# Performance work log

Measured on AMD Instinct MI355X. Metric: run time of the kernel, lower is better.

The kernel has to match this reference:

```python
import jax, jax.numpy as jnp
import numpy as np

D = 2048      # hidden_size
H = 16        # num_attention_heads
KV = 4        # num_key_value_heads
HD = 128      # head_dim
E = 16        # num_experts
TOPK = 2      # num_experts_per_tok
I = 768       # moe_intermediate_size
EPS = 1e-6
THETA = 1000000.0


def rms_norm(x, w, eps=EPS):
    x32 = x.astype(jnp.float32)
    y = x32 * jax.lax.rsqrt(jnp.mean(x32 * x32, axis=-1, keepdims=True) + eps)
    return (y.astype(x.dtype)) * w


def rotate_half(x):
    x1, x2 = jnp.split(x, 2, axis=-1)
    return jnp.concatenate([-x2, x1], axis=-1)


def rope_cos_sin(position_ids):
    inv_freq = 1.0 / (THETA ** (jnp.arange(0, HD, 2, dtype=jnp.float32) / HD))
    ang = position_ids.astype(jnp.float32)[..., None] * inv_freq   # [B,S,HD/2]
    emb = jnp.concatenate([ang, ang], axis=-1)                     # [B,S,HD]
    return jnp.cos(emb)[:, None, :, :], jnp.sin(emb)[:, None, :, :]  # [B,1,S,HD]


def setup_inputs() -> dict:
    key = jax.random.key(0)
    ks = jax.random.split(key, 10)
    s = 0.02
    B, S = 1, 1024
    return {
        "hidden_states": jax.random.normal(ks[0], (B, S, D), jnp.float32),
        "ln1_w": jnp.ones((D,), jnp.float32),
        "ln2_w": jnp.ones((D,), jnp.float32),
        "qn_w": jnp.ones((HD,), jnp.float32),
        "kn_w": jnp.ones((HD,), jnp.float32),
        "Wq": jax.random.normal(ks[1], (H * HD, D), jnp.float32) * s,
        "Wk": jax.random.normal(ks[2], (KV * HD, D), jnp.float32) * s,
        "Wv": jax.random.normal(ks[3], (KV * HD, D), jnp.float32) * s,
        "Wo": jax.random.normal(ks[4], (D, H * HD), jnp.float32) * s,
        "gate_w": jax.random.normal(ks[5], (E, D), jnp.float32) * s,
        "Wg": jax.random.normal(ks[6], (E, I, D), jnp.float32) * s,
        "Wu": jax.random.normal(ks[7], (E, I, D), jnp.float32) * s,
        "Wd": jax.random.normal(ks[8], (E, D, I), jnp.float32) * s,
        "position_ids": jnp.arange(S, dtype=jnp.int32)[None, :],
    }


def attention(h, qn_w, kn_w, Wq, Wk, Wv, Wo, position_ids):
    B, S, _ = h.shape
    q = (h @ Wq.T).reshape(B, S, H, HD)
    k = (h @ Wk.T).reshape(B, S, KV, HD)
    v = (h @ Wv.T).reshape(B, S, KV, HD)
    q = rms_norm(q, qn_w).transpose(0, 2, 1, 3)   # [B,H,S,HD]
    k = rms_norm(k, kn_w).transpose(0, 2, 1, 3)   # [B,KV,S,HD]
    v = v.transpose(0, 2, 1, 3)
    cos, sin = rope_cos_sin(position_ids)
    q = q * cos + rotate_half(q) * sin
    k = k * cos + rotate_half(k) * sin
    # repeat_kv (GQA): expand KV heads to H heads
    rep = H // KV
    k = jnp.repeat(k, rep, axis=1)
    v = jnp.repeat(v, rep, axis=1)
    scale = HD ** -0.5
    scores = jnp.einsum('bhqd,bhkd->bhqk', q, k) * scale
    probs = jax.nn.softmax(scores.astype(jnp.float32), axis=-1).astype(q.dtype)
    out = jnp.einsum('bhqk,bhkd->bhqd', probs, v)
    out = out.transpose(0, 2, 1, 3).reshape(B, S, H * HD)
    return out @ Wo.T


def moe(h, gate_w, Wg, Wu, Wd):
    B, S, _ = h.shape
    x = h.reshape(-1, D)                                  # [T,D]
    T = x.shape[0]
    logits = x @ gate_w.T                                 # [T,E]
    probs = jax.nn.softmax(logits.astype(jnp.float32), axis=-1)
    w, sel = jax.lax.top_k(probs, TOPK)                   # [T,K]
    w = w / jnp.sum(w, axis=-1, keepdims=True)            # norm_topk_prob
    combine = jnp.zeros((T, E), jnp.float32).at[jnp.arange(T)[:, None], sel].add(w)
    g = jnp.einsum('td,eid->tei', x, Wg)                  # [T,E,I]
    u = jnp.einsum('td,eid->tei', x, Wu)
    a = jax.nn.silu(g) * u
    y = jnp.einsum('tei,edi->ted', a, Wd)                 # [T,E,D]
    out = jnp.einsum('ted,te->td', y, combine.astype(x.dtype))
    return out.reshape(B, S, D)


def reference(hidden_states, ln1_w, ln2_w, qn_w, kn_w, Wq, Wk, Wv, Wo, gate_w, Wg, Wu, Wd, position_ids):
    # pre-attn RMSNorm -> bidirectional GQA attention -> residual
    residual = hidden_states
    h = rms_norm(hidden_states, ln1_w)
    h = residual + attention(h, qn_w, kn_w, Wq, Wk, Wv, Wo, position_ids)
    # post-attn RMSNorm -> top-k sparse MoE -> residual
    residual = h
    h2 = rms_norm(h, ln2_w)
    return residual + moe(h2, gate_w, Wg, Wu, Wd)
```

## Files before the change

kernel.cpp:

```cpp
#include <hip/hip_runtime.h>
#include <hip/hip_bf16.h>
#include <math.h>

#define D 2048
#define NH 16
#define NKV 4
#define HD 128
#define NE 16
#define NI 768
#define S 1024
#define EPS 1e-6f

typedef __attribute__((ext_vector_type(8))) short bf16x8;
typedef __attribute__((ext_vector_type(4))) float f32x4;

__device__ __forceinline__ float wave_reduce_sum64(float v) {
    for (int off = 32; off; off >>= 1) v += __shfl_xor(v, off, 64);
    return v;
}

__device__ __forceinline__ unsigned short f2bf(float f) {
    unsigned int x = __float_as_uint(f);
    x += 0x7FFFu + ((x >> 16) & 1u);
    return (unsigned short)(x >> 16);
}

__device__ __forceinline__ bf16x8 pack8(const float4 a, const float4 b) {
    bf16x8 r;
    r[0] = (short)f2bf(a.x); r[1] = (short)f2bf(a.y);
    r[2] = (short)f2bf(a.z); r[3] = (short)f2bf(a.w);
    r[4] = (short)f2bf(b.x); r[5] = (short)f2bf(b.y);
    r[6] = (short)f2bf(b.z); r[7] = (short)f2bf(b.w);
    return r;
}

__global__ void rmsnorm_kernel(const float* __restrict__ x, const float* __restrict__ w,
                               float* __restrict__ y, unsigned short* __restrict__ yb) {
    int t = blockIdx.x;
    const float* xr = x + (size_t)t * D;
    float* yr = y + (size_t)t * D;
    float v[8];
    float ss = 0.f;
#pragma unroll
    for (int m = 0; m < 8; ++m) {
        v[m] = xr[threadIdx.x + 256 * m];
        ss += v[m] * v[m];
    }
    ss = wave_reduce_sum64(ss);
    __shared__ float wsum[4];
    if ((threadIdx.x & 63) == 0) wsum[threadIdx.x >> 6] = ss;
    __syncthreads();
    float tot = wsum[0] + wsum[1] + wsum[2] + wsum[3];
    float r = rsqrtf(tot / (float)D + EPS);
#pragma unroll
    for (int m = 0; m < 8; ++m) {
        int d = threadIdx.x + 256 * m;
        float val = v[m] * r * w[d];
        yr[d] = val;
        if (yb) yb[(size_t)t * D + d] = f2bf(val);
    }
}

__global__ __launch_bounds__(256) void mfma_gemm_kernel(
    const float* __restrict__ A, int lda,
    const float* __restrict__ W, int ldw,
    float* __restrict__ C, int ldc,
    const float* __restrict__ R, float* __restrict__ C2,
    int M, int N, int K)
{
    int m0 = blockIdx.y * 64;
    int n0 = blockIdx.x * 64;

    __shared__ unsigned short As[64 * 64];
    __shared__ unsigned short Bs[64 * 64];

    int tid = threadIdx.x;
    int srow = tid >> 2;
    int scol = (tid & 3) * 16;

    const float* ap = A + (size_t)(m0 + srow) * lda + scol;
    const float* wp = W + (size_t)(n0 + srow) * ldw + scol;

    int wlo[2];
#pragma unroll
    for (int u = 0; u < 2; ++u) {
        int g = (tid & 3) * 2 + u;
        wlo[u] = srow * 64 + (g ^ (srow & 7)) * 8;
    }

    int wid = tid >> 6, lane = tid & 63;
    int wm = wid >> 1, wn = wid & 1;
    int l16 = lane & 15, lhi = lane >> 4;

    int ra[2][2], rb[2][2];
#pragma unroll
    for (int f = 0; f < 2; ++f) {
        int rowa = wm * 32 + f * 16 + l16;
        int rowb = wn * 32 + f * 16 + l16;
#pragma unroll
        for (int kh = 0; kh < 2; ++kh) {
            ra[f][kh] = rowa * 64 + (((kh * 4 + lhi) ^ (rowa & 7))) * 8;
            rb[f][kh] = rowb * 64 + (((kh * 4 + lhi) ^ (rowb & 7))) * 8;
        }
    }

    f32x4 acc[2][2] = {};
    float4 av[4], wv[4];

    auto ldt = [&](int k0) {
#pragma unroll
        for (int u = 0; u < 4; ++u) {
            av[u] = *(const float4*)(ap + k0 + u * 4);
            wv[u] = *(const float4*)(wp + k0 + u * 4);
        }
    };

    ldt(0);
    for (int k0 = 0; k0 < K; k0 += 64) {
        bf16x8 pa0 = pack8(av[0], av[1]);
        bf16x8 pa1 = pack8(av[2], av[3]);
        bf16x8 pw0 = pack8(wv[0], wv[1]);
        bf16x8 pw1 = pack8(wv[2], wv[3]);
        __syncthreads();
        *(bf16x8*)(As + wlo[0]) = pa0;
        *(bf16x8*)(As + wlo[1]) = pa1;
        *(bf16x8*)(Bs + wlo[0]) = pw0;
        *(bf16x8*)(Bs + wlo[1]) = pw1;
        __syncthreads();
        if (k0 + 64 < K) ldt(k0 + 64);
#pragma unroll
        for (int kh = 0; kh < 2; ++kh) {
            bf16x8 af0 = *(const bf16x8*)(As + ra[0][kh]);
            bf16x8 af1 = *(const bf16x8*)(As + ra[1][kh]);
            bf16x8 bf0 = *(const bf16x8*)(Bs + rb[0][kh]);
            bf16x8 bf1 = *(const bf16x8*)(Bs + rb[1][kh]);
            acc[0][0] = __builtin_amdgcn_mfma_f32_16x16x32_bf16(af0, bf0, acc[0][0], 0, 0, 0);
            acc[0][1] = __builtin_amdgcn_mfma_f32_16x16x32_bf16(af0, bf1, acc[0][1], 0, 0, 0);
            acc[1][0] = __builtin_amdgcn_mfma_f32_16x16x32_bf16(af1, bf0, acc[1][0], 0, 0, 0);
            acc[1][1] = __builtin_amdgcn_mfma_f32_16x16x32_bf16(af1, bf1, acc[1][1], 0, 0, 0);
        }
    }

#pragma unroll
    for (int mi = 0; mi < 2; ++mi) {
#pragma unroll
        for (int r = 0; r < 4; ++r) {
            int grow = m0 + wm * 32 + mi * 16 + lhi * 4 + r;
#pragma unroll
            for (int ni = 0; ni < 2; ++ni) {
                int gcol = n0 + wn * 32 + ni * 16 + l16;
                float v = acc[mi][ni][r];
                if (R) v += R[(size_t)grow * ldc + gcol];
                C[(size_t)grow * ldc + gcol] = v;
                if (C2) C2[(size_t)grow * ldc + gcol] = v;
            }
        }
    }
}

__global__ __launch_bounds__(256) void qkv_gemm_kernel(
    const float* __restrict__ A,
    const float* __restrict__ Wq, const float* __restrict__ Wk, const float* __restrict__ Wv,
    float* __restrict__ C)
{
    int m0 = blockIdx.y * 64;
    int n0 = blockIdx.x * 64;

    const float* W;
    int wr0;
    if (n0 < 2048)      { W = Wq; wr0 = n0; }
    else if (n0 < 2560) { W = Wk; wr0 = n0 - 2048; }
    else                { W = Wv; wr0 = n0 - 2560; }

    __shared__ unsigned short As[64 * 64];
    __shared__ unsigned short Bs[64 * 64];

    int tid = threadIdx.x;
    int srow = tid >> 2;
    int scol = (tid & 3) * 16;

    const float* ap = A + (size_t)(m0 + srow) * D + scol;
    const float* wp = W + (size_t)(wr0 + srow) * D + scol;

    int wlo[2];
#pragma unroll
    for (int u = 0; u < 2; ++u) {
        int g = (tid & 3) * 2 + u;
        wlo[u] = srow * 64 + (g ^ (srow & 7)) * 8;
    }

    int wid = tid >> 6, lane = tid & 63;
    int wm = wid >> 1, wn = wid & 1;
    int l16 = lane & 15, lhi = lane >> 4;

    int ra[2][2], rb[2][2];
#pragma unroll
    for (int f = 0; f < 2; ++f) {
        int rowa = wm * 32 + f * 16 + l16;
        int rowb = wn * 32 + f * 16 + l16;
#pragma unroll
        for (int kh = 0; kh < 2; ++kh) {
            ra[f][kh] = rowa * 64 + (((kh * 4 + lhi) ^ (rowa & 7))) * 8;
            rb[f][kh] = rowb * 64 + (((kh * 4 + lhi) ^ (rowb & 7))) * 8;
        }
    }

    f32x4 acc[2][2] = {};
    float4 av[4], wv[4];

    auto ldt = [&](int k0) {
#pragma unroll
        for (int u = 0; u < 4; ++u) {
            av[u] = *(const float4*)(ap + k0 + u * 4);
            wv[u] = *(const float4*)(wp + k0 + u * 4);
        }
    };

    ldt(0);
    for (int k0 = 0; k0 < D; k0 += 64) {
        bf16x8 pa0 = pack8(av[0], av[1]);
        bf16x8 pa1 = pack8(av[2], av[3]);
        bf16x8 pw0 = pack8(wv[0], wv[1]);
        bf16x8 pw1 = pack8(wv[2], wv[3]);
        __syncthreads();
        *(bf16x8*)(As + wlo[0]) = pa0;
        *(bf16x8*)(As + wlo[1]) = pa1;
        *(bf16x8*)(Bs + wlo[0]) = pw0;
        *(bf16x8*)(Bs + wlo[1]) = pw1;
        __syncthreads();
        if (k0 + 64 < D) ldt(k0 + 64);
#pragma unroll
        for (int kh = 0; kh < 2; ++kh) {
            bf16x8 af0 = *(const bf16x8*)(As + ra[0][kh]);
            bf16x8 af1 = *(const bf16x8*)(As + ra[1][kh]);
            bf16x8 bf0 = *(const bf16x8*)(Bs + rb[0][kh]);
            bf16x8 bf1 = *(const bf16x8*)(Bs + rb[1][kh]);
            acc[0][0] = __builtin_amdgcn_mfma_f32_16x16x32_bf16(af0, bf0, acc[0][0], 0, 0, 0);
            acc[0][1] = __builtin_amdgcn_mfma_f32_16x16x32_bf16(af0, bf1, acc[0][1], 0, 0, 0);
            acc[1][0] = __builtin_amdgcn_mfma_f32_16x16x32_bf16(af1, bf0, acc[1][0], 0, 0, 0);
            acc[1][1] = __builtin_amdgcn_mfma_f32_16x16x32_bf16(af1, bf1, acc[1][1], 0, 0, 0);
        }
    }

#pragma unroll
    for (int mi = 0; mi < 2; ++mi) {
#pragma unroll
        for (int r = 0; r < 4; ++r) {
            int grow = m0 + wm * 32 + mi * 16 + lhi * 4 + r;
#pragma unroll
            for (int ni = 0; ni < 2; ++ni) {
                int gcol = n0 + wn * 32 + ni * 16 + l16;
                C[(size_t)grow * 3072 + gcol] = acc[mi][ni][r];
            }
        }
    }
}

__global__ __launch_bounds__(256) void moe_mlp_kernel(
    const unsigned short* __restrict__ h2b,
    const float* __restrict__ Wg, const float* __restrict__ Wu,
    const int* __restrict__ cnt, const int* __restrict__ elist,
    unsigned short* __restrict__ abuf)
{
    int e = blockIdx.z;
    int me = cnt[e];
    int m0 = blockIdx.y * 64;
    if (m0 >= me) return;
    int n0 = blockIdx.x * 16;

    __shared__ unsigned short As[64 * 64];
    __shared__ unsigned short Gs[16 * 64];
    __shared__ unsigned short Us[16 * 64];
    __shared__ int ridx[64];

    int tid = threadIdx.x;
    const int* idx = elist + e * S;
    if (tid < 64) ridx[tid] = (m0 + tid < me) ? idx[m0 + tid] : -1;
    __syncthreads();

    int arow_i = tid >> 2;
    int acolg = (tid & 3) * 16;
    int rva = ridx[arow_i];
    const unsigned short* arow = (rva >= 0) ? (h2b + (size_t)(rva >> 1) * D + acolg) : nullptr;
    int wa[2];
#pragma unroll
    for (int u = 0; u < 2; ++u) {
        int g = (tid & 3) * 2 + u;
        wa[u] = arow_i * 64 + (g ^ (arow_i & 7)) * 8;
    }

    int tl = tid & 127;
    int bwrow = tl >> 3;
    int bg8 = tl & 7;
    const float* bp = ((tid < 128) ? Wg : Wu) + ((size_t)e * NI + n0 + bwrow) * D + bg8 * 8;
    unsigned short* bs = (tid < 128) ? Gs : Us;
    int wbo = bwrow * 64 + (bg8 ^ (bwrow & 7)) * 8;

    int wid = tid >> 6, lane = tid & 63;
    int l16 = lane & 15, lhi = lane >> 4;

    int raoff[2], rboff[2];
    {
        int rowa = wid * 16 + l16;
#pragma unroll
        for (int kh = 0; kh < 2; ++kh) {
            raoff[kh] = rowa * 64 + (((kh * 4 + lhi) ^ (rowa & 7))) * 8;
            rboff[kh] = l16 * 64 + (((kh * 4 + lhi) ^ (l16 & 7))) * 8;
        }
    }

    f32x4 accg = {}, accu = {};
    bf16x8 av[2];
    float4 bv[2];

    auto ldt = [&](int k0) {
        if (arow) {
            av[0] = *(const bf16x8*)(arow + k0);
            av[1] = *(const bf16x8*)(arow + k0 + 8);
        } else {
            bf16x8 z = {};
            av[0] = z; av[1] = z;
        }
        bv[0] = *(const float4*)(bp + k0);
        bv[1] = *(const float4*)(bp + k0 + 4);
    };

    ldt(0);
    for (int k0 = 0; k0 < D; k0 += 64) {
        bf16x8 a0s = av[0], a1s = av[1];
        bf16x8 pb = pack8(bv[0], bv[1]);
        __syncthreads();
        *(bf16x8*)(As + wa[0]) = a0s;
        *(bf16x8*)(As + wa[1]) = a1s;
        *(bf16x8*)(bs + wbo) = pb;
        __syncthreads();
        if (k0 + 64 < D) ldt(k0 + 64);
#pragma unroll
        for (int kh = 0; kh < 2; ++kh) {
            bf16x8 a = *(const bf16x8*)(As + raoff[kh]);
            bf16x8 bgf = *(const bf16x8*)(Gs + rboff[kh]);
            bf16x8 buf = *(const bf16x8*)(Us + rboff[kh]);
            accg = __builtin_amdgcn_mfma_f32_16x16x32_bf16(a, bgf, accg, 0, 0, 0);
            accu = __builtin_amdgcn_mfma_f32_16x16x32_bf16(a, buf, accu, 0, 0, 0);
        }
    }

#pragma unroll
    for (int r = 0; r < 4; ++r) {
        int lrow = wid * 16 + lhi * 4 + r;
        int rv = ridx[lrow];
        if (rv < 0) continue;
        float g = accg[r];
        float u = accu[r];
        float a = g / (1.f + __expf(-g)) * u;
        abuf[(size_t)rv * NI + n0 + l16] = f2bf(a);
    }
}

__global__ __launch_bounds__(256) void moe_down_kernel(
    const unsigned short* __restrict__ abuf, const float* __restrict__ Wd,
    const int* __restrict__ cnt, const int* __restrict__ elist,
    const float* __restrict__ wbuf, float* __restrict__ out)
{
    int e = blockIdx.z;
    int me = cnt[e];
    int m0 = blockIdx.y * 64;
    if (m0 >= me) return;
    int n0 = blockIdx.x * 16;

    __shared__ unsigned short As[64 * 64];
    __shared__ unsigned short Bs[16 * 64];
    __shared__ int ridx[64];

    int tid = threadIdx.x;
    const int* idx = elist + e * S;
    if (tid < 64) ridx[tid] = (m0 + tid < me) ? idx[m0 + tid] : -1;
    __syncthreads();

    int arow_i = tid >> 2;
    int acolg = (tid & 3) * 16;
    int rva = ridx[arow_i];
    const unsigned short* arow = (rva >= 0) ? (abuf + (size_t)rva * NI + acolg) : nullptr;
    int wa[2];
#pragma unroll
    for (int u = 0; u < 2; ++u) {
        int g = (tid & 3) * 2 + u;
        wa[u] = arow_i * 64 + (g ^ (arow_i & 7)) * 8;
    }

    int tl = tid & 127;
    int bwrow = tl >> 3;
    int bg8 = tl & 7;
    const float* bp = Wd + ((size_t)e * D + n0 + bwrow) * NI + bg8 * 8;
    int wbo = bwrow * 64 + (bg8 ^ (bwrow & 7)) * 8;
    bool doB = tid < 128;

    int wid = tid >> 6, lane = tid & 63;
    int l16 = lane & 15, lhi = lane >> 4;

    int raoff[2], rboff[2];
    {
        int rowa = wid * 16 + l16;
#pragma unroll
        for (int kh = 0; kh < 2; ++kh) {
            raoff[kh] = rowa * 64 + (((kh * 4 + lhi) ^ (rowa & 7))) * 8;
            rboff[kh] = l16 * 64 + (((kh * 4 + lhi) ^ (l16 & 7))) * 8;
        }
    }

    f32x4 acc = {};
    bf16x8 av[2];
    float4 bv[2];

    auto ldt = [&](int k0) {
        if (arow) {
            av[0] = *(const bf16x8*)(arow + k0);
            av[1] = *(const bf16x8*)(arow + k0 + 8);
        } else {
            bf16x8 z = {};
            av[0] = z; av[1] = z;
        }
        if (doB) {
            bv[0] = *(const float4*)(bp + k0);
            bv[1] = *(const float4*)(bp + k0 + 4);
        }
    };

    ldt(0);
    for (int k0 = 0; k0 < NI; k0 += 64) {
        bf16x8 a0s = av[0], a1s = av[1];
        bf16x8 pb = pack8(bv[0], bv[1]);
        __syncthreads();
        *(bf16x8*)(As + wa[0]) = a0s;
        *(bf16x8*)(As + wa[1]) = a1s;
        if (doB) *(bf16x8*)(Bs + wbo) = pb;
        __syncthreads();
        if (k0 + 64 < NI) ldt(k0 + 64);
#pragma unroll
        for (int kh = 0; kh < 2; ++kh) {
            bf16x8 a = *(const bf16x8*)(As + raoff[kh]);
            bf16x8 b = *(const bf16x8*)(Bs + rboff[kh]);
            acc = __builtin_amdgcn_mfma_f32_16x16x32_bf16(a, b, acc, 0, 0, 0);
        }
    }

#pragma unroll
    for (int r = 0; r < 4; ++r) {
        int lrow = wid * 16 + lhi * 4 + r;
        int rv = ridx[lrow];
        if (rv < 0) continue;
        float w = wbuf[rv];
        atomicAdd(out + (size_t)(rv >> 1) * D + n0 + l16, w * acc[r]);
    }
}

__global__ void qkrope_bf16_kernel(const float* __restrict__ qkvb,
                                   const float* __restrict__ qn_w, const float* __restrict__ kn_w,
                                   const int* __restrict__ pos_ids,
                                   unsigned short* __restrict__ qbh, unsigned short* __restrict__ kbh)
{
    int t = blockIdx.x;
    int h = blockIdx.y;
    int d = threadIdx.x;
    const float* base;
    const float* w;
    unsigned short* ob;
    float scale;
    if (h < NH) {
        base = qkvb + (size_t)t * 3072 + h * HD; w = qn_w;
        ob = qbh + (size_t)t * D + h * HD; scale = 0.08838834764831845f;
    } else {
        base = qkvb + (size_t)t * 3072 + 2048 + (h - NH) * HD; w = kn_w;
        ob = kbh + (size_t)t * (NKV * HD) + (h - NH) * HD; scale = 1.0f;
    }
    float x1 = base[d], x2 = base[d + 64];
    float ss = wave_reduce_sum64(x1 * x1 + x2 * x2);
    float r = rsqrtf(ss / (float)HD + EPS);
    float n1 = x1 * r * w[d];
    float n2 = x2 * r * w[d + 64];
    float pos = (float)pos_ids[t];
    float freq = powf(1000000.0f, -(float)d * (1.0f / 64.0f));
    float ang = pos * freq;
    float c, s;
    sincosf(ang, &s, &c);
    ob[d]      = f2bf((n1 * c - n2 * s) * scale);
    ob[d + 64] = f2bf((n2 * c + n1 * s) * scale);
}

__global__ void vtrans_kernel(const float* __restrict__ qkvb, unsigned short* __restrict__ vbt)
{
    __shared__ unsigned short tile[64][65];
    int s0 = blockIdx.x * 64, d0 = blockIdx.y * 64, kvh = blockIdx.z;
    int tid = threadIdx.x;
    {
        int i = tid >> 2;
        int j4 = (tid & 3) * 16;
        const float* src = qkvb + (size_t)(s0 + i) * 3072 + 2560 + kvh * HD + d0 + j4;
#pragma unroll
        for (int u = 0; u < 4; ++u) {
            float4 f = *(const float4*)(src + u * 4);
            tile[i][j4 + u * 4 + 0] = f2bf(f.x);
            tile[i][j4 + u * 4 + 1] = f2bf(f.y);
            tile[i][j4 + u * 4 + 2] = f2bf(f.z);
            tile[i][j4 + u * 4 + 3] = f2bf(f.w);
        }
    }
    __syncthreads();
    {
        int j = tid >> 2;
        int i4 = (tid & 3) * 16;
        bf16x8 o0, o1;
#pragma unroll
        for (int u = 0; u < 8; ++u) {
            o0[u] = (short)tile[i4 + u][j];
            o1[u] = (short)tile[i4 + 8 + u][j];
        }
        unsigned short* dst = vbt + ((size_t)kvh * HD + d0 + j) * S + s0 + i4;
        *(bf16x8*)(dst) = o0;
        *(bf16x8*)(dst + 8) = o1;
    }
}

__global__ __launch_bounds__(256) void flash_attn_mfma_kernel(
    const unsigned short* __restrict__ qbh, const unsigned short* __restrict__ kbh,
    const unsigned short* __restrict__ vbt, float* __restrict__ o)
{
    int qt = blockIdx.x;
    int h  = blockIdx.y;
    int kvh = h >> 2;

    __shared__ unsigned short Qs[64 * 128];
    __shared__ unsigned short Ks[64 * 128];
    __shared__ unsigned short Vs[128 * 64];
    __shared__ unsigned short Ps[4][16 * 72];

    int tid = threadIdx.x;
    int wid = tid >> 6, lane = tid & 63;
    int l16 = lane & 15, lhi = lane >> 4;

    {
        int r = tid >> 2;
        int gb = (tid & 3) * 4;
        const unsigned short* src = qbh + (size_t)(qt * 64 + r) * D + h * HD;
#pragma unroll
        for (int u = 0; u < 4; ++u) {
            int g = gb + u;
            bf16x8 val = *(const bf16x8*)(src + g * 8);
            *(bf16x8*)(Qs + r * 128 + (g ^ (r & 7)) * 8) = val;
        }
    }

    int qrow = wid * 16 + l16;
    int qoff[4];
#pragma unroll
    for (int kh = 0; kh < 4; ++kh)
        qoff[kh] = qrow * 128 + (((kh * 4 + lhi) ^ (qrow & 7))) * 8;

    float mreg[4], lreg[4];
#pragma unroll
    for (int r = 0; r < 4; ++r) { mreg[r] = -3.0e38f; lreg[r] = 0.f; }
    f32x4 oacc[8] = {};

    for (int kt = 0; kt < S / 64; ++kt) {
        __syncthreads();
        {
            int r = tid >> 2;
            int gb = (tid & 3) * 4;
            const unsigned short* src = kbh + (size_t)(kt * 64 + r) * (NKV * HD) + kvh * HD;
#pragma unroll
            for (int u = 0; u < 4; ++u) {
                int g = gb + u;
                bf16x8 val = *(const bf16x8*)(src + g * 8);
                *(bf16x8*)(Ks + r * 128 + (g ^ (r & 7)) * 8) = val;
            }
        }
        {
            int r = tid >> 1;
            int gb = (tid & 1) * 4;
            const unsigned short* src = vbt + ((size_t)kvh * HD + r) * S + kt * 64;
#pragma unroll
            for (int u = 0; u < 4; ++u) {
                int g = gb + u;
                bf16x8 val = *(const bf16x8*)(src + g * 8);
                *(bf16x8*)(Vs + r * 64 + (g ^ (r & 7)) * 8) = val;
            }
        }
        __syncthreads();

        bf16x8 qa[4];
#pragma unroll
        for (int kh = 0; kh < 4; ++kh) qa[kh] = *(const bf16x8*)(Qs + qoff[kh]);
        f32x4 sc[4] = {};
#pragma unroll
        for (int nf = 0; nf < 4; ++nf) {
            int krow = nf * 16 + l16;
#pragma unroll
            for (int kh = 0; kh < 4; ++kh) {
                bf16x8 kf = *(const bf16x8*)(Ks + krow * 128 + (((kh * 4 + lhi) ^ (krow & 7))) * 8);
                sc[nf] = __builtin_amdgcn_mfma_f32_16x16x32_bf16(qa[kh], kf, sc[nf], 0, 0, 0);
            }
        }

        float corr[4];
#pragma unroll
        for (int r = 0; r < 4; ++r) {
            float tmax = fmaxf(fmaxf(sc[0][r], sc[1][r]), fmaxf(sc[2][r], sc[3][r]));
            tmax = fmaxf(tmax, __shfl_xor(tmax, 1, 64));
            tmax = fmaxf(tmax, __shfl_xor(tmax, 2, 64));
            tmax = fmaxf(tmax, __shfl_xor(tmax, 4, 64));
            tmax = fmaxf(tmax, __shfl_xor(tmax, 8, 64));
            float mn = fmaxf(mreg[r], tmax);
            corr[r] = __expf(mreg[r] - mn);
            mreg[r] = mn;
            float psum = 0.f;
#pragma unroll
            for (int nf = 0; nf < 4; ++nf) {
                float p = __expf(sc[nf][r] - mn);
                sc[nf][r] = p;
                psum += p;
            }
            psum += __shfl_xor(psum, 1, 64);
            psum += __shfl_xor(psum, 2, 64);
            psum += __shfl_xor(psum, 4, 64);
            psum += __shfl_xor(psum, 8, 64);
            lreg[r] = lreg[r] * corr[r] + psum;
        }
#pragma unroll
        for (int fb = 0; fb < 8; ++fb)
#pragma unroll
            for (int r = 0; r < 4; ++r) oacc[fb][r] *= corr[r];

#pragma unroll
        for (int nf = 0; nf < 4; ++nf)
#pragma unroll
            for (int r = 0; r < 4; ++r)
                Ps[wid][(lhi * 4 + r) * 72 + nf * 16 + l16] = f2bf(sc[nf][r]);

        bf16x8 pa[2];
#pragma unroll
        for (int k2 = 0; k2 < 2; ++k2)
            pa[k2] = *(const bf16x8*)(&Ps[wid][l16 * 72 + k2 * 32 + lhi * 8]);

#pragma unroll
        for (int fb = 0; fb < 8; ++fb) {
            int vrow = fb * 16 + l16;
#pragma unroll
            for (int k2 = 0; k2 < 2; ++k2) {
                bf16x8 vf = *(const bf16x8*)(Vs + vrow * 64 + (((k2 * 4 + lhi) ^ (vrow & 7))) * 8);
                oacc[fb] = __builtin_amdgcn_mfma_f32_16x16x32_bf16(pa[k2], vf, oacc[fb], 0, 0, 0);
            }
        }
    }

    float linv[4];
#pragma unroll
    for (int r = 0; r < 4; ++r) linv[r] = 1.f / lreg[r];
#pragma unroll
    for (int fb = 0; fb < 8; ++fb) {
#pragma unroll
        for (int r = 0; r < 4; ++r) {
            int row = qt * 64 + wid * 16 + lhi * 4 + r;
            o[(size_t)row * D + h * HD + fb * 16 + l16] = oacc[fb][r] * linv[r];
        }
    }
}

__global__ void gate_kernel(const float* __restrict__ x, const float* __restrict__ gw,
                            float* __restrict__ wbuf, int* __restrict__ cnt, int* __restrict__ elist)
{
    int t = blockIdx.x;
    int g = threadIdx.x >> 4, j = threadIdx.x & 15;
    const float* xr = x + (size_t)t * D;
    const float* gr = gw + (size_t)g * D;
    float p = 0.f;
    for (int m = 0; m < D / 16; ++m) p += xr[j + 16 * m] * gr[j + 16 * m];
    for (int off = 8; off; off >>= 1) p += __shfl_down(p, off, 64);
    __shared__ float lg[NE];
    if (j == 0) lg[g] = p;
    __syncthreads();
    if (threadIdx.x == 0) {
        float l0 = -1e30f; int i0 = 0;
        for (int e = 0; e < NE; ++e) if (lg[e] > l0) { l0 = lg[e]; i0 = e; }
        float l1 = -1e30f; int i1 = 0;
        for (int e = 0; e < NE; ++e) if (e != i0 && lg[e] > l1) { l1 = lg[e]; i1 = e; }
        float rr = expf(l1 - l0);
        wbuf[t * 2 + 0] = 1.f / (1.f + rr);
        wbuf[t * 2 + 1] = rr / (1.f + rr);
        int s0 = atomicAdd(&cnt[i0], 1); elist[i0 * S + s0] = t * 2;
        int s1 = atomicAdd(&cnt[i1], 1); elist[i1 * S + s1] = t * 2 + 1;
    }
}

extern "C" void kernel_launch(void* const* d_in, const int* in_sizes, int n_in,
                              void* d_out, int out_size, void* d_ws, size_t ws_size,
                              hipStream_t stream)
{
    const float* hidden = (const float*)d_in[0];
    const float* ln1 = (const float*)d_in[1];
    const float* ln2 = (const float*)d_in[2];
    const float* qn  = (const float*)d_in[3];
    const float* kn  = (const float*)d_in[4];
    const float* Wq  = (const float*)d_in[5];
    const float* Wk  = (const float*)d_in[6];
    const float* Wv  = (const float*)d_in[7];
    const float* Wo  = (const float*)d_in[8];
    const float* gw  = (const float*)d_in[9];
    const float* Wg  = (const float*)d_in[10];
    const float* Wu  = (const float*)d_in[11];
    const float* Wd  = (const float*)d_in[12];
    const int*   pos = (const int*)d_in[13];

    float* ws    = (float*)d_ws;
    float* h1    = ws;
    float* qkvb  = h1 + 2097152;
    float* attn  = qkvb + 3145728;
    float* hattn = attn + 2097152;
    float* h2    = hattn + 2097152;
    float* h2bf  = h2 + 2097152;
    float* wbuf  = h2bf + 1048576;
    int*   cnt   = (int*)(wbuf + 2048);
    int*   elist = cnt + 16;

    unsigned short* qbh = (unsigned short*)h1;
    unsigned short* kbh = (unsigned short*)(h1 + 1048576);
    unsigned short* vbt = (unsigned short*)(h1 + 1310720);
    unsigned short* abuf = (unsigned short*)attn;
    unsigned short* h2b  = (unsigned short*)h2bf;
    float* out   = (float*)d_out;

    hipMemsetAsync(cnt, 0, NE * sizeof(int), stream);

    rmsnorm_kernel<<<S, 256, 0, stream>>>(hidden, ln1, h1, nullptr);
    qkv_gemm_kernel<<<dim3(48, 16), 256, 0, stream>>>(h1, Wq, Wk, Wv, qkvb);
    qkrope_bf16_kernel<<<dim3(S, NH + NKV), 64, 0, stream>>>(qkvb, qn, kn, pos, qbh, kbh);
    vtrans_kernel<<<dim3(S / 64, HD / 64, NKV), 256, 0, stream>>>(qkvb, vbt);
    flash_attn_mfma_kernel<<<dim3(S / 64, NH), 256, 0, stream>>>(qbh, kbh, vbt, attn);
    mfma_gemm_kernel<<<dim3(32, 16), 256, 0, stream>>>(attn, D, Wo, D, hattn, D, hidden, out, S, 2048, D);
    rmsnorm_kernel<<<S, 256, 0, stream>>>(hattn, ln2, h2, h2b);
    gate_kernel<<<S, 256, 0, stream>>>(h2, gw, wbuf, cnt, elist);
    moe_mlp_kernel<<<dim3(NI / 16, 16, NE), 256, 0, stream>>>(h2b, Wg, Wu, cnt, elist, abuf);
    moe_down_kernel<<<dim3(D / 16, 16, NE), 256, 0, stream>>>(abuf, Wd, cnt, elist, wbuf, out);
}
```

Baseline: 342.3 us.

## Double-buffer LDS tiles in all GEMM kernels with one barrier per stage

Converts the generic, QKV, MoE gate/up and MoE down GEMM kernels to ping-pong LDS buffers with two register sets of prefetched global loads, processing two K-tiles per loop iteration. This removes one of the two __syncthreads per K-step and issues the next global load earlier, so memory latency overlaps the MFMAs. In exchange it doubles LDS use and adds prefetch registers, which may lower occupancy. It also assumes K is a multiple of 128, which holds for 2048 and 768.

```diff
diff --git a/kernel.cpp b/kernel.cpp
--- a/kernel.cpp
+++ b/kernel.cpp
@@ -71,8 +71,8 @@
     int m0 = blockIdx.y * 64;
     int n0 = blockIdx.x * 64;
 
-    __shared__ unsigned short As[64 * 64];
-    __shared__ unsigned short Bs[64 * 64];
+    __shared__ unsigned short As[2][64 * 64];
+    __shared__ unsigned short Bs[2][64 * 64];
 
     int tid = threadIdx.x;
     int srow = tid >> 2;
@@ -105,40 +105,49 @@
     }
 
     f32x4 acc[2][2] = {};
-    float4 av[4], wv[4];
-
-    auto ldt = [&](int k0) {
+    float4 avA[4], wvA[4], avB[4], wvB[4];
+
+    auto ldt = [&](float4* av, float4* wv, int k0) {
 #pragma unroll
         for (int u = 0; u < 4; ++u) {
             av[u] = *(const float4*)(ap + k0 + u * 4);
             wv[u] = *(const float4*)(wp + k0 + u * 4);
         }
     };
-
-    ldt(0);
-    for (int k0 = 0; k0 < K; k0 += 64) {
+    auto stage = [&](const float4* av, const float4* wv, int b) {
         bf16x8 pa0 = pack8(av[0], av[1]);
         bf16x8 pa1 = pack8(av[2], av[3]);
         bf16x8 pw0 = pack8(wv[0], wv[1]);
         bf16x8 pw1 = pack8(wv[2], wv[3]);
-        __syncthreads();
-        *(bf16x8*)(As + wlo[0]) = pa0;
-        *(bf16x8*)(As + wlo[1]) = pa1;
-        *(bf16x8*)(Bs + wlo[0]) = pw0;
-        *(bf16x8*)(Bs + wlo[1]) = pw1;
-        __syncthreads();
-        if (k0 + 64 < K) ldt(k0 + 64);
+        *(bf16x8*)(&As[b][wlo[0]]) = pa0;
+        *(bf16x8*)(&As[b][wlo[1]]) = pa1;
+        *(bf16x8*)(&Bs[b][wlo[0]]) = pw0;
+        *(bf16x8*)(&Bs[b][wlo[1]]) = pw1;
+    };
+    auto domfma = [&](int b) {
 #pragma unroll
         for (int kh = 0; kh < 2; ++kh) {
-            bf16x8 af0 = *(const bf16x8*)(As + ra[0][kh]);
-            bf16x8 af1 = *(const bf16x8*)(As + ra[1][kh]);
-            bf16x8 bf0 = *(const bf16x8*)(Bs + rb[0][kh]);
-            bf16x8 bf1 = *(const bf16x8*)(Bs + rb[1][kh]);
+            bf16x8 af0 = *(const bf16x8*)(&As[b][ra[0][kh]]);
+            bf16x8 af1 = *(const bf16x8*)(&As[b][ra[1][kh]]);
+            bf16x8 bf0 = *(const bf16x8*)(&Bs[b][rb[0][kh]]);
+            bf16x8 bf1 = *(const bf16x8*)(&Bs[b][rb[1][kh]]);
             acc[0][0] = __builtin_amdgcn_mfma_f32_16x16x32_bf16(af0, bf0, acc[0][0], 0, 0, 0);
             acc[0][1] = __builtin_amdgcn_mfma_f32_16x16x32_bf16(af0, bf1, acc[0][1], 0, 0, 0);
             acc[1][0] = __builtin_amdgcn_mfma_f32_16x16x32_bf16(af1, bf0, acc[1][0], 0, 0, 0);
             acc[1][1] = __builtin_amdgcn_mfma_f32_16x16x32_bf16(af1, bf1, acc[1][1], 0, 0, 0);
         }
+    };
+
+    ldt(avA, wvA, 0);
+    for (int k0 = 0; k0 < K; k0 += 128) {
+        ldt(avB, wvB, k0 + 64);
+        stage(avA, wvA, 0);
+        __syncthreads();
+        domfma(0);
+        if (k0 + 128 < K) ldt(avA, wvA, k0 + 128);
+        stage(avB, wvB, 1);
+        __syncthreads();
+        domfma(1);
     }
 
 #pragma unroll
@@ -172,8 +181,8 @@
     else if (n0 < 2560) { W = Wk; wr0 = n0 - 2048; }
     else                { W = Wv; wr0 = n0 - 2560; }
 
-    __shared__ unsigned short As[64 * 64];
-    __shared__ unsigned short Bs[64 * 64];
+    __shared__ unsigned short As[2][64 * 64];
+    __shared__ unsigned short Bs[2][64 * 64];
 
     int tid = threadIdx.x;
     int srow = tid >> 2;
@@ -206,40 +215,49 @@
     }
 
     f32x4 acc[2][2] = {};
-    float4 av[4], wv[4];
-
-    auto ldt = [&](int k0) {
+    float4 avA[4], wvA[4], avB[4], wvB[4];
+
+    auto ldt = [&](float4* av, float4* wv, int k0) {
 #pragma unroll
         for (int u = 0; u < 4; ++u) {
             av[u] = *(const float4*)(ap + k0 + u * 4);
             wv[u] = *(const float4*)(wp + k0 + u * 4);
         }
     };
-
-    ldt(0);
-    for (int k0 = 0; k0 < D; k0 += 64) {
+    auto stage = [&](const float4* av, const float4* wv, int b) {
         bf16x8 pa0 = pack8(av[0], av[1]);
         bf16x8 pa1 = pack8(av[2], av[3]);
         bf16x8 pw0 = pack8(wv[0], wv[1]);
         bf16x8 pw1 = pack8(wv[2], wv[3]);
-        __syncthreads();
-        *(bf16x8*)(As + wlo[0]) = pa0;
-        *(bf16x8*)(As + wlo[1]) = pa1;
-        *(bf16x8*)(Bs + wlo[0]) = pw0;
-        *(bf16x8*)(Bs + wlo[1]) = pw1;
-        __syncthreads();
-        if (k0 + 64 < D) ldt(k0 + 64);
+        *(bf16x8*)(&As[b][wlo[0]]) = pa0;
+        *(bf16x8*)(&As[b][wlo[1]]) = pa1;
+        *(bf16x8*)(&Bs[b][wlo[0]]) = pw0;
+        *(bf16x8*)(&Bs[b][wlo[1]]) = pw1;
+    };
+    auto domfma = [&](int b) {
 #pragma unroll
         for (int kh = 0; kh < 2; ++kh) {
-            bf16x8 af0 = *(const bf16x8*)(As + ra[0][kh]);
-            bf16x8 af1 = *(const bf16x8*)(As + ra[1][kh]);
-            bf16x8 bf0 = *(const bf16x8*)(Bs + rb[0][kh]);
-            bf16x8 bf1 = *(const bf16x8*)(Bs + rb[1][kh]);
+            bf16x8 af0 = *(const bf16x8*)(&As[b][ra[0][kh]]);
+            bf16x8 af1 = *(const bf16x8*)(&As[b][ra[1][kh]]);
+            bf16x8 bf0 = *(const bf16x8*)(&Bs[b][rb[0][kh]]);
+            bf16x8 bf1 = *(const bf16x8*)(&Bs[b][rb[1][kh]]);
             acc[0][0] = __builtin_amdgcn_mfma_f32_16x16x32_bf16(af0, bf0, acc[0][0], 0, 0, 0);
             acc[0][1] = __builtin_amdgcn_mfma_f32_16x16x32_bf16(af0, bf1, acc[0][1], 0, 0, 0);
             acc[1][0] = __builtin_amdgcn_mfma_f32_16x16x32_bf16(af1, bf0, acc[1][0], 0, 0, 0);
             acc[1][1] = __builtin_amdgcn_mfma_f32_16x16x32_bf16(af1, bf1, acc[1][1], 0, 0, 0);
         }
+    };
+
+    ldt(avA, wvA, 0);
+    for (int k0 = 0; k0 < D; k0 += 128) {
+        ldt(avB, wvB, k0 + 64);
+        stage(avA, wvA, 0);
+        __syncthreads();
+        domfma(0);
+        if (k0 + 128 < D) ldt(avA, wvA, k0 + 128);
+        stage(avB, wvB, 1);
+        __syncthreads();
+        domfma(1);
     }
 
 #pragma unroll
@@ -268,9 +286,9 @@
     if (m0 >= me) return;
     int n0 = blockIdx.x * 16;
 
-    __shared__ unsigned short As[64 * 64];
-    __shared__ unsigned short Gs[16 * 64];
-    __shared__ unsigned short Us[16 * 64];
+    __shared__ unsigned short As[2][64 * 64];
+    __shared__ unsigned short Gs[2][16 * 64];
+    __shared__ unsigned short Us[2][16 * 64];
     __shared__ int ridx[64];
 
     int tid = threadIdx.x;
@@ -293,8 +311,8 @@
     int bwrow = tl >> 3;
     int bg8 = tl & 7;
     const float* bp = ((tid < 128) ? Wg : Wu) + ((size_t)e * NI + n0 + bwrow) * D + bg8 * 8;
-    unsigned short* bs = (tid < 128) ? Gs : Us;
     int wbo = bwrow * 64 + (bg8 ^ (bwrow & 7)) * 8;
+    bool isG = tid < 128;
 
     int wid = tid >> 6, lane = tid & 63;
     int l16 = lane & 15, lhi = lane >> 4;
@@ -310,10 +328,10 @@
     }
 
     f32x4 accg = {}, accu = {};
-    bf16x8 av[2];
-    float4 bv[2];
-
-    auto ldt = [&](int k0) {
+    bf16x8 avA[2], avB[2];
+    float4 bvA[2], bvB[2];
+
+    auto ldt = [&](bf16x8* av, float4* bv, int k0) {
         if (arow) {
             av[0] = *(const bf16x8*)(arow + k0);
             av[1] = *(const bf16x8*)(arow + k0 + 8);
@@ -324,25 +342,34 @@
         bv[0] = *(const float4*)(bp + k0);
         bv[1] = *(const float4*)(bp + k0 + 4);
     };
-
-    ldt(0);
-    for (int k0 = 0; k0 < D; k0 += 64) {
-        bf16x8 a0s = av[0], a1s = av[1];
+    auto stage = [&](const bf16x8* av, const float4* bv, int b) {
         bf16x8 pb = pack8(bv[0], bv[1]);
-        __syncthreads();
-        *(bf16x8*)(As + wa[0]) = a0s;
-        *(bf16x8*)(As + wa[1]) = a1s;
-        *(bf16x8*)(bs + wbo) = pb;
-        __syncthreads();
-        if (k0 + 64 < D) ldt(k0 + 64);
+        *(bf16x8*)(&As[b][wa[0]]) = av[0];
+        *(bf16x8*)(&As[b][wa[1]]) = av[1];
+        if (isG) *(bf16x8*)(&Gs[b][wbo]) = pb;
+        else     *(bf16x8*)(&Us[b][wbo]) = pb;
+    };
+    auto domfma = [&](int b) {
 #pragma unroll
         for (int kh = 0; kh < 2; ++kh) {
-            bf16x8 a = *(const bf16x8*)(As + raoff[kh]);
-            bf16x8 bgf = *(const bf16x8*)(Gs + rboff[kh]);
-            bf16x8 buf = *(const bf16x8*)(Us + rboff[kh]);
+            bf16x8 a = *(const bf16x8*)(&As[b][raoff[kh]]);
+            bf16x8 bgf = *(const bf16x8*)(&Gs[b][rboff[kh]]);
+            bf16x8 buf = *(const bf16x8*)(&Us[b][rboff[kh]]);
             accg = __builtin_amdgcn_mfma_f32_16x16x32_bf16(a, bgf, accg, 0, 0, 0);
             accu = __builtin_amdgcn_mfma_f32_16x16x32_bf16(a, buf, accu, 0, 0, 0);
         }
+    };
+
+    ldt(avA, bvA, 0);
+    for (int k0 = 0; k0 < D; k0 += 128) {
+        ldt(avB, bvB, k0 + 64);
+        stage(avA, bvA, 0);
+        __syncthreads();
+        domfma(0);
+        if (k0 + 128 < D) ldt(avA, bvA, k0 + 128);
+        stage(avB, bvB, 1);
+        __syncthreads();
+        domfma(1);
     }
 
 #pragma unroll
@@ -368,8 +395,8 @@
     if (m0 >= me) return;
     int n0 = blockIdx.x * 16;
 
-    __shared__ unsigned short As[64 * 64];
-    __shared__ unsigned short Bs[16 * 64];
+    __shared__ unsigned short As[2][64 * 64];
+    __shared__ unsigned short Bs[2][16 * 64];
     __shared__ int ridx[64];
 
     int tid = threadIdx.x;
@@ -409,10 +436,10 @@
     }
 
     f32x4 acc = {};
-    bf16x8 av[2];
-    float4 bv[2];
-
-    auto ldt = [&](int k0) {
+    bf16x8 avA[2], avB[2];
+    float4 bvA[2], bvB[2];
+
+    auto ldt = [&](bf16x8* av, float4* bv, int k0) {
         if (arow) {
             av[0] = *(const bf16x8*)(arow + k0);
             av[1] = *(const bf16x8*)(arow + k0 + 8);
@@ -425,23 +452,33 @@
             bv[1] = *(const float4*)(bp + k0 + 4);
         }
     };
-
-    ldt(0);
-    for (int k0 = 0; k0 < NI; k0 += 64) {
-        bf16x8 a0s = av[0], a1s = av[1];
-        bf16x8 pb = pack8(bv[0], bv[1]);
-        __syncthreads();
-        *(bf16x8*)(As + wa[0]) = a0s;
-        *(bf16x8*)(As + wa[1]) = a1s;
-        if (doB) *(bf16x8*)(Bs + wbo) = pb;
-        __syncthreads();
-        if (k0 + 64 < NI) ldt(k0 + 64);
+    auto stage = [&](const bf16x8* av, const float4* bv, int b) {
+        *(bf16x8*)(&As[b][wa[0]]) = av[0];
+        *(bf16x8*)(&As[b][wa[1]]) = av[1];
+        if (doB) {
+            bf16x8 pb = pack8(bv[0], bv[1]);
+            *(bf16x8*)(&Bs[b][wbo]) = pb;
+        }
+    };
+    auto domfma = [&](int b) {
 #pragma unroll
         for (int kh = 0; kh < 2; ++kh) {
-            bf16x8 a = *(const bf16x8*)(As + raoff[kh]);
-            bf16x8 b = *(const bf16x8*)(Bs + rboff[kh]);
-            acc = __builtin_amdgcn_mfma_f32_16x16x32_bf16(a, b, acc, 0, 0, 0);
-        }
+            bf16x8 a = *(const bf16x8*)(&As[b][raoff[kh]]);
+            bf16x8 bb = *(const bf16x8*)(&Bs[b][rboff[kh]]);
+            acc = __builtin_amdgcn_mfma_f32_16x16x32_bf16(a, bb, acc, 0, 0, 0);
+        }
+    };
+
+    ldt(avA, bvA, 0);
+    for (int k0 = 0; k0 < NI; k0 += 128) {
+        ldt(avB, bvB, k0 + 64);
+        stage(avA, bvA, 0);
+        __syncthreads();
+        domfma(0);
+        if (k0 + 128 < NI) ldt(avA, bvA, k0 + 128);
+        stage(avB, bvB, 1);
+        __syncthreads();
+        domfma(1);
     }
 
 #pragma unroll
```

After: 336.8 us. No clear change (-1.6%).

## Double-buffer LDS in dense GEMMs and stagger K-loop start per block

Applied to the files above, without the earlier changes.

The generic and QKV GEMM kernels now use two LDS buffers with a two-stage software pipeline, which cuts one barrier per K step and lets global loads overlap the MFMA work. All GEMM-style kernels, including the MoE gate/up and down kernels, also rotate the K iteration start by a per-block offset. The offset spreads concurrent blocks across different memory regions to reduce channel or cache contention. The cost is double the LDS per block and more registers for the two load sets, which may lower occupancy. The generic GEMM pipeline assumes NS is even.

```diff
diff --git a/kernel.cpp b/kernel.cpp
--- a/kernel.cpp
+++ b/kernel.cpp
@@ -70,9 +70,11 @@
 {
     int m0 = blockIdx.y * 64;
     int n0 = blockIdx.x * 64;
-
-    __shared__ unsigned short As[64 * 64];
-    __shared__ unsigned short Bs[64 * 64];
+    int NS = K >> 6;
+    int off = (blockIdx.x * 7 + blockIdx.y * 13) % NS;
+
+    __shared__ unsigned short As[2][64 * 64];
+    __shared__ unsigned short Bs[2][64 * 64];
 
     int tid = threadIdx.x;
     int srow = tid >> 2;
@@ -104,41 +106,56 @@
         }
     }
 
+    auto kof = [&](int s) {
+        int t = s + off;
+        if (t >= NS) t -= NS;
+        return t << 6;
+    };
+
     f32x4 acc[2][2] = {};
-    float4 av[4], wv[4];
-
-    auto ldt = [&](int k0) {
+    float4 avA[4], wvA[4], avB[4], wvB[4];
+
+    auto ldt = [&](float4* av, float4* wv, int k0) {
 #pragma unroll
         for (int u = 0; u < 4; ++u) {
             av[u] = *(const float4*)(ap + k0 + u * 4);
             wv[u] = *(const float4*)(wp + k0 + u * 4);
         }
     };
-
-    ldt(0);
-    for (int k0 = 0; k0 < K; k0 += 64) {
+    auto stage = [&](const float4* av, const float4* wv, int b) {
         bf16x8 pa0 = pack8(av[0], av[1]);
         bf16x8 pa1 = pack8(av[2], av[3]);
         bf16x8 pw0 = pack8(wv[0], wv[1]);
         bf16x8 pw1 = pack8(wv[2], wv[3]);
-        __syncthreads();
-        *(bf16x8*)(As + wlo[0]) = pa0;
-        *(bf16x8*)(As + wlo[1]) = pa1;
-        *(bf16x8*)(Bs + wlo[0]) = pw0;
-        *(bf16x8*)(Bs + wlo[1]) = pw1;
-        __syncthreads();
-        if (k0 + 64 < K) ldt(k0 + 64);
+        *(bf16x8*)(&As[b][wlo[0]]) = pa0;
+        *(bf16x8*)(&As[b][wlo[1]]) = pa1;
+        *(bf16x8*)(&Bs[b][wlo[0]]) = pw0;
+        *(bf16x8*)(&Bs[b][wlo[1]]) = pw1;
+    };
+    auto domfma = [&](int b) {
 #pragma unroll
         for (int kh = 0; kh < 2; ++kh) {
-            bf16x8 af0 = *(const bf16x8*)(As + ra[0][kh]);
-            bf16x8 af1 = *(const bf16x8*)(As + ra[1][kh]);
-            bf16x8 bf0 = *(const bf16x8*)(Bs + rb[0][kh]);
-            bf16x8 bf1 = *(const bf16x8*)(Bs + rb[1][kh]);
+            bf16x8 af0 = *(const bf16x8*)(&As[b][ra[0][kh]]);
+            bf16x8 af1 = *(const bf16x8*)(&As[b][ra[1][kh]]);
+            bf16x8 bf0 = *(const bf16x8*)(&Bs[b][rb[0][kh]]);
+            bf16x8 bf1 = *(const bf16x8*)(&Bs[b][rb[1][kh]]);
             acc[0][0] = __builtin_amdgcn_mfma_f32_16x16x32_bf16(af0, bf0, acc[0][0], 0, 0, 0);
             acc[0][1] = __builtin_amdgcn_mfma_f32_16x16x32_bf16(af0, bf1, acc[0][1], 0, 0, 0);
             acc[1][0] = __builtin_amdgcn_mfma_f32_16x16x32_bf16(af1, bf0, acc[1][0], 0, 0, 0);
             acc[1][1] = __builtin_amdgcn_mfma_f32_16x16x32_bf16(af1, bf1, acc[1][1], 0, 0, 0);
         }
+    };
+
+    ldt(avA, wvA, kof(0));
+    for (int s = 0; s < NS; s += 2) {
+        ldt(avB, wvB, kof(s + 1));
+        stage(avA, wvA, 0);
+        __syncthreads();
+        domfma(0);
+        if (s + 2 < NS) ldt(avA, wvA, kof(s + 2));
+        stage(avB, wvB, 1);
+        __syncthreads();
+        domfma(1);
     }
 
 #pragma unroll
@@ -165,6 +182,7 @@
 {
     int m0 = blockIdx.y * 64;
     int n0 = blockIdx.x * 64;
+    int off = (blockIdx.x * 7 + blockIdx.y * 13) & 31;
 
     const float* W;
     int wr0;
@@ -172,8 +190,8 @@
     else if (n0 < 2560) { W = Wk; wr0 = n0 - 2048; }
     else                { W = Wv; wr0 = n0 - 2560; }
 
-    __shared__ unsigned short As[64 * 64];
-    __shared__ unsigned short Bs[64 * 64];
+    __shared__ unsigned short As[2][64 * 64];
+    __shared__ unsigned short Bs[2][64 * 64];
 
     int tid = threadIdx.x;
     int srow = tid >> 2;
@@ -205,41 +223,52 @@
         }
     }
 
+    auto kof = [&](int s) { return ((s + off) & 31) << 6; };
+
     f32x4 acc[2][2] = {};
-    float4 av[4], wv[4];
-
-    auto ldt = [&](int k0) {
+    float4 avA[4], wvA[4], avB[4], wvB[4];
+
+    auto ldt = [&](float4* av, float4* wv, int k0) {
 #pragma unroll
         for (int u = 0; u < 4; ++u) {
             av[u] = *(const float4*)(ap + k0 + u * 4);
             wv[u] = *(const float4*)(wp + k0 + u * 4);
         }
     };
-
-    ldt(0);
-    for (int k0 = 0; k0 < D; k0 += 64) {
+    auto stage = [&](const float4* av, const float4* wv, int b) {
         bf16x8 pa0 = pack8(av[0], av[1]);
         bf16x8 pa1 = pack8(av[2], av[3]);
         bf16x8 pw0 = pack8(wv[0], wv[1]);
         bf16x8 pw1 = pack8(wv[2], wv[3]);
-        __syncthreads();
-        *(bf16x8*)(As + wlo[0]) = pa0;
-        *(bf16x8*)(As + wlo[1]) = pa1;
-        *(bf16x8*)(Bs + wlo[0]) = pw0;
-        *(bf16x8*)(Bs + wlo[1]) = pw1;
-        __syncthreads();
-        if (k0 + 64 < D) ldt(k0 + 64);
+        *(bf16x8*)(&As[b][wlo[0]]) = pa0;
+        *(bf16x8*)(&As[b][wlo[1]]) = pa1;
+        *(bf16x8*)(&Bs[b][wlo[0]]) = pw0;
+        *(bf16x8*)(&Bs[b][wlo[1]]) = pw1;
+    };
+    auto domfma = [&](int b) {
 #pragma unroll
         for (int kh = 0; kh < 2; ++kh) {
-            bf16x8 af0 = *(const bf16x8*)(As + ra[0][kh]);
-            bf16x8 af1 = *(const bf16x8*)(As + ra[1][kh]);
-            bf16x8 bf0 = *(const bf16x8*)(Bs + rb[0][kh]);
-            bf16x8 bf1 = *(const bf16x8*)(Bs + rb[1][kh]);
+            bf16x8 af0 = *(const bf16x8*)(&As[b][ra[0][kh]]);
+            bf16x8 af1 = *(const bf16x8*)(&As[b][ra[1][kh]]);
+            bf16x8 bf0 = *(const bf16x8*)(&Bs[b][rb[0][kh]]);
+            bf16x8 bf1 = *(const bf16x8*)(&Bs[b][rb[1][kh]]);
             acc[0][0] = __builtin_amdgcn_mfma_f32_16x16x32_bf16(af0, bf0, acc[0][0], 0, 0, 0);
             acc[0][1] = __builtin_amdgcn_mfma_f32_16x16x32_bf16(af0, bf1, acc[0][1], 0, 0, 0);
             acc[1][0] = __builtin_amdgcn_mfma_f32_16x16x32_bf16(af1, bf0, acc[1][0], 0, 0, 0);
             acc[1][1] = __builtin_amdgcn_mfma_f32_16x16x32_bf16(af1, bf1, acc[1][1], 0, 0, 0);
         }
+    };
+
+    ldt(avA, wvA, kof(0));
+    for (int s = 0; s < 32; s += 2) {
+        ldt(avB, wvB, kof(s + 1));
+        stage(avA, wvA, 0);
+        __syncthreads();
+        domfma(0);
+        if (s + 2 < 32) ldt(avA, wvA, kof(s + 2));
+        stage(avB, wvB, 1);
+        __syncthreads();
+        domfma(1);
     }
 
 #pragma unroll
@@ -267,6 +296,7 @@
     int m0 = blockIdx.y * 64;
     if (m0 >= me) return;
     int n0 = blockIdx.x * 16;
+    int off = (blockIdx.x * 7 + blockIdx.y * 13 + blockIdx.z * 11) & 31;
 
     __shared__ unsigned short As[64 * 64];
     __shared__ unsigned short Gs[16 * 64];
@@ -308,6 +338,8 @@
             rboff[kh] = l16 * 64 + (((kh * 4 + lhi) ^ (l16 & 7))) * 8;
         }
     }
+
+    auto kof = [&](int s) { return ((s + off) & 31) << 6; };
 
     f32x4 accg = {}, accu = {};
     bf16x8 av[2];
@@ -325,8 +357,8 @@
         bv[1] = *(const float4*)(bp + k0 + 4);
     };
 
-    ldt(0);
-    for (int k0 = 0; k0 < D; k0 += 64) {
+    ldt(kof(0));
+    for (int s = 0; s < 32; ++s) {
         bf16x8 a0s = av[0], a1s = av[1];
         bf16x8 pb = pack8(bv[0], bv[1]);
         __syncthreads();
@@ -334,7 +366,7 @@
         *(bf16x8*)(As + wa[1]) = a1s;
         *(bf16x8*)(bs + wbo) = pb;
         __syncthreads();
-        if (k0 + 64 < D) ldt(k0 + 64);
+        if (s + 1 < 32) ldt(kof(s + 1));
 #pragma unroll
         for (int kh = 0; kh < 2; ++kh) {
             bf16x8 a = *(const bf16x8*)(As + raoff[kh]);
@@ -367,6 +399,7 @@
     int m0 = blockIdx.y * 64;
     if (m0 >= me) return;
     int n0 = blockIdx.x * 16;
+    int off = (blockIdx.x * 5 + blockIdx.y * 7 + blockIdx.z * 3) % 12;
 
     __shared__ unsigned short As[64 * 64];
     __shared__ unsigned short Bs[16 * 64];
@@ -407,6 +440,12 @@
             rboff[kh] = l16 * 64 + (((kh * 4 + lhi) ^ (l16 & 7))) * 8;
         }
     }
+
+    auto kof = [&](int s) {
+        int t = s + off;
+        if (t >= 12) t -= 12;
+        return t << 6;
+    };
 
     f32x4 acc = {};
     bf16x8 av[2];
@@ -426,8 +465,8 @@
         }
     };
 
-    ldt(0);
-    for (int k0 = 0; k0 < NI; k0 += 64) {
+    ldt(kof(0));
+    for (int s = 0; s < 12; ++s) {
         bf16x8 a0s = av[0], a1s = av[1];
         bf16x8 pb = pack8(bv[0], bv[1]);
         __syncthreads();
@@ -435,7 +474,7 @@
         *(bf16x8*)(As + wa[1]) = a1s;
         if (doB) *(bf16x8*)(Bs + wbo) = pb;
         __syncthreads();
-        if (k0 + 64 < NI) ldt(k0 + 64);
+        if (s + 1 < 12) ldt(kof(s + 1));
 #pragma unroll
         for (int kh = 0; kh < 2; ++kh) {
             bf16x8 a = *(const bf16x8*)(As + raoff[kh]);
```

Measured after the change: 395.7 us. 1.16x slower.
